# Optimization experiments

Measured on AMD Instinct MI355X. Metric: run time of the kernel, lower is better.

## Reference

```python
import jax, jax.numpy as jnp
import numpy as np

N_QUBITS = 16
DIM = 1 << N_QUBITS
NUM_CLASSES = 23
BATCH = 64

# PauliZ sign table: wire 0 is the most-significant bit of the flattened index.
_idx = np.arange(DIM)
SIGNS = np.stack([1 - 2 * ((_idx >> (N_QUBITS - 1 - w)) & 1) for w in range(N_QUBITS)], axis=1).astype(np.float32)  # (DIM, 16)


def _rx_mat(theta):
    c = jnp.cos(theta / 2).astype(jnp.complex64)
    s = (-1j * jnp.sin(theta / 2)).astype(jnp.complex64)
    return jnp.stack([jnp.stack([c, s]), jnp.stack([s, c])])  # (2,2)


def _rot_mat(phi, theta, omega):
    ct = jnp.cos(theta / 2)
    st = jnp.sin(theta / 2)
    a = jnp.exp(-0.5j * (phi + omega)) * ct
    b = -jnp.exp(0.5j * (phi - omega)) * st
    c = jnp.exp(-0.5j * (phi - omega)) * st
    d = jnp.exp(0.5j * (phi + omega)) * ct
    return jnp.stack([jnp.stack([a, b]), jnp.stack([c, d])]).astype(jnp.complex64)


def _apply_1q(state, U, w):
    # state: (B, 2,...,2); shared 2x2 gate on wire w (axis w+1)
    st = jnp.tensordot(state, U, axes=[[w + 1], [1]])  # contracted axis moves to last
    return jnp.moveaxis(st, -1, w + 1)


def _apply_rx_batched(state, theta_b, w):
    # per-sample RX angles theta_b: (B,)
    half = theta_b / 2
    c = jnp.cos(half).astype(jnp.complex64)
    s = (-1j * jnp.sin(half)).astype(jnp.complex64)
    U = jnp.stack([jnp.stack([c, s], -1), jnp.stack([s, c], -1)], -2)  # (B,2,2)
    st = jnp.moveaxis(state, w + 1, -1)
    st = jnp.einsum('bji,b...i->b...j', U, st)
    return jnp.moveaxis(st, -1, w + 1)


def _apply_crx(state, theta, ctrl, tgt):
    s0 = jax.lax.index_in_dim(state, 0, axis=ctrl + 1, keepdims=False)
    s1 = jax.lax.index_in_dim(state, 1, axis=ctrl + 1, keepdims=False)
    tax = tgt + 1 if tgt < ctrl else tgt  # target axis after control axis removal
    U = _rx_mat(theta)
    s1 = jnp.moveaxis(jnp.tensordot(s1, U, axes=[[tax], [1]]), -1, tax)
    return jnp.stack([s0, s1], axis=ctrl + 1)


def _circuit(x, w0, x0, w1, x1):
    B = x.shape[0]
    state = jnp.zeros((B,) + (2,) * N_QUBITS, jnp.complex64)
    state = state.at[(slice(None),) + (0,) * N_QUBITS].set(1.0)
    for w, xc in ((w0, x0), (w1, x1)):
        for q in range(N_QUBITS):
            state = _apply_rx_batched(state, x[:, q], q)
        for q in range(N_QUBITS):
            state = _apply_1q(state, _rot_mat(w[q, 0], w[q, 1], w[q, 2]), q)
        for q in range(N_QUBITS):
            state = _apply_crx(state, xc[q], q, (q + 1) % N_QUBITS)
    probs = (state.real ** 2 + state.imag ** 2).reshape(B, DIM)
    return probs @ jnp.asarray(SIGNS)  # (B, 16) PauliZ expvals


def setup_inputs() -> dict:
    key = jax.random.key(0)
    ks = jax.random.split(key, 7)
    return {
        'x': jax.random.normal(ks[0], (BATCH, N_QUBITS), jnp.float32),
        'w0': jax.random.normal(ks[1], (N_QUBITS, 3), jnp.float32),
        'x0': jax.random.normal(ks[2], (N_QUBITS,), jnp.float32),
        'w1': jax.random.normal(ks[3], (N_QUBITS, 3), jnp.float32),
        'x1': jax.random.normal(ks[4], (N_QUBITS,), jnp.float32),
        'fc_w': jax.random.normal(ks[5], (NUM_CLASSES, N_QUBITS), jnp.float32) * 0.25,
        'fc_b': jax.random.normal(ks[6], (NUM_CLASSES,), jnp.float32) * 0.05,
    }


def reference(x, w0, x0, w1, x1, fc_w, fc_b):
    feats = _circuit(x, w0, x0, w1, x1)           # (B, 16)
    logits = feats @ fc_w.T + fc_b                # (B, 23)
    return jax.nn.log_softmax(logits, axis=1)
```

## Files before the change

### kernel.cpp

```cpp
#include <hip/hip_runtime.h>
#include <hip/hip_bf16.h>


#define DIM 65536
#define BATCH 64
#define PSTR 580


template<int RB>
__device__ __forceinline__ void g1q_reg(float* sr, float* si, const float* U) {
  float u00r=U[0],u00i=U[1],u01r=U[2],u01i=U[3],u10r=U[4],u10i=U[5],u11r=U[6],u11i=U[7];
#pragma unroll
  for (int k = 0; k < 8; ++k) {
    int lo = k & ((1<<RB)-1);
    int j0 = ((k >> RB) << (RB+1)) | lo;
    int j1 = j0 | (1<<RB);
    float a0r=sr[j0], a0i=si[j0], a1r=sr[j1], a1i=si[j1];
    sr[j0] = u00r*a0r - u00i*a0i + u01r*a1r - u01i*a1i;
    si[j0] = u00r*a0i + u00i*a0r + u01r*a1i + u01i*a1r;
    sr[j1] = u10r*a0r - u10i*a0i + u11r*a1r - u11i*a1i;
    si[j1] = u10r*a0i + u10i*a0r + u11r*a1i + u11i*a1r;
  }
}

template<int RB, int CB>
__device__ __forceinline__ void gsel_reg_cc(float* sr, float* si, const float* M0, const float* M1) {
  float a0=M0[0],a1=M0[1],a2=M0[2],a3=M0[3],a4=M0[4],a5=M0[5],a6=M0[6],a7=M0[7];
  float b0=M1[0],b1=M1[1],b2=M1[2],b3=M1[3],b4=M1[4],b5=M1[5],b6=M1[6],b7=M1[7];
#pragma unroll
  for (int k = 0; k < 8; ++k) {
    int lo = k & ((1<<RB)-1);
    int j0 = ((k >> RB) << (RB+1)) | lo;
    int j1 = j0 | (1<<RB);
    const bool c = ((j0 >> CB) & 1) != 0;
    float u00r=c?b0:a0, u00i=c?b1:a1, u01r=c?b2:a2, u01i=c?b3:a3;
    float u10r=c?b4:a4, u10i=c?b5:a5, u11r=c?b6:a6, u11i=c?b7:a7;
    float p0r=sr[j0], p0i=si[j0], p1r=sr[j1], p1i=si[j1];
    sr[j0] = u00r*p0r - u00i*p0i + u01r*p1r - u01i*p1i;
    si[j0] = u00r*p0i + u00i*p0r + u01r*p1i + u01i*p1r;
    sr[j1] = u10r*p0r - u10i*p0i + u11r*p1r - u11i*p1i;
    si[j1] = u10r*p0i + u10i*p0r + u11r*p1i + u11i*p1r;
  }
}

template<int RB>
__device__ __forceinline__ void gsel_reg_pred(float* sr, float* si, const float* M0,
                                              const float* M1, bool ctrl) {
  float u[8];
#pragma unroll
  for (int e = 0; e < 8; ++e) u[e] = ctrl ? M1[e] : M0[e];
  g1q_reg<RB>(sr, si, u);
}

template<int CB, int LB>
__device__ __forceinline__ void crx_reg_lane(float* sr, float* si, float c, float s) {
#pragma unroll
  for (int k = 0; k < 8; ++k) {
    int lo2 = k & ((1<<CB)-1);
    int j = ((((k >> CB) << (CB+1)) | lo2)) | (1<<CB);
    float pr = __shfl_xor(sr[j], 1<<LB, 64);
    float pi = __shfl_xor(si[j], 1<<LB, 64);
    float mr = sr[j], mi = si[j];
    sr[j] = c*mr + s*pi;
    si[j] = c*mi - s*pr;
  }
}

__device__ __forceinline__ int swz(int o) { return o ^ ((o>>4)&15) ^ ((o>>8)&15); }

__device__ __forceinline__ unsigned bfp(float r, float i) {
  unsigned ur = __float_as_uint(r), ui = __float_as_uint(i);
  ur = (ur + 0x7fffu + ((ur >> 16) & 1u)) >> 16;
  ui = (ui + 0x7fffu + ((ui >> 16) & 1u)) & 0xffff0000u;
  return (ur & 0xffffu) | ui;
}
__device__ __forceinline__ float bfr(unsigned u) { return __uint_as_float(u << 16); }
__device__ __forceinline__ float bfi(unsigned u) { return __uint_as_float(u & 0xffff0000u); }

#define MP(Pb, l, q, s) ((Pb) + (((l)*16+(q))*2+(s))*8)


__global__ __launch_bounds__(512) void pB(unsigned* __restrict__ st,
                                          const float* __restrict__ x, const float* __restrict__ w0,
                                          const float* __restrict__ x0, const float* __restrict__ w1,
                                          const float* __restrict__ x1, float* __restrict__ P,
                                          float* __restrict__ feats, int* __restrict__ ctr) {
  __shared__ float2 lds2[8192];
  __shared__ float Ps[PSTR];
  int blk = blockIdx.x;
  int b = blk >> 3, m = blk & 7;
  int t = threadIdx.x, lane = t & 63, wv = t >> 6;

  {
    float (*su)[8] = reinterpret_cast<float(*)[8]>(lds2);
    if (m == 0 && t < 16) feats[b*16 + t] = 0.f;
    if (m == 0 && t == 16) ctr[b] = 0;
    if (t < 32) {
      int l = t >> 4, q = t & 15;
      const float* W = (l ? w1 : w0) + q*3;
      float xa = 0.5f * x[b*16 + q];
      float cr = cosf(xa), sx = sinf(xa);
      float phi = W[0], th = W[1], om = W[2];
      float ct = cosf(0.5f*th), stt = sinf(0.5f*th);
      float po = 0.5f*(phi+om), pm = 0.5f*(phi-om);
      float ar =  cosf(po)*ct,  ai = -sinf(po)*ct;
      float br = -cosf(pm)*stt, bi = -sinf(pm)*stt;
      float cr2 = cosf(pm)*stt, ci2 = -sinf(pm)*stt;
      float dr =  cosf(po)*ct,  di =  sinf(po)*ct;
      float U[8];
      U[0] = ar*cr + bi*sx;   U[1] = ai*cr - br*sx;
      U[2] = ai*sx + br*cr;   U[3] = -ar*sx + bi*cr;
      U[4] = cr2*cr + di*sx;  U[5] = ci2*cr - dr*sx;
      U[6] = ci2*sx + dr*cr;  U[7] = -cr2*sx + di*cr;
      float* M0 = MP(Ps, l, q, 0);
      float* M1 = M0 + 8;
#pragma unroll
      for (int e = 0; e < 8; ++e) { M0[e] = U[e]; su[t][e] = U[e]; }
      if (q == 0) {
        float ang = l ? 0.5f*x0[15] : 0.f;
        float cg = cosf(ang), sg = sinf(ang);
        M1[0] =  cg*U[0] + sg*U[3];  M1[1] = cg*U[1] - sg*U[2];
        M1[2] =  sg*U[1] + cg*U[2];  M1[3] = -sg*U[0] + cg*U[3];
        M1[4] =  cg*U[4] + sg*U[7];  M1[5] = cg*U[5] - sg*U[6];
        M1[6] =  sg*U[5] + cg*U[6];  M1[7] = -sg*U[4] + cg*U[7];
      } else {
        float ang = 0.5f*(l ? x1[q-1] : x0[q-1]);
        float cg = cosf(ang), sg = sinf(ang);
        M1[0] = cg*U[0] + sg*U[5];  M1[1] = cg*U[1] - sg*U[4];
        M1[2] = cg*U[2] + sg*U[7];  M1[3] = cg*U[3] - sg*U[6];
        M1[4] = cg*U[4] + sg*U[1];  M1[5] = cg*U[5] - sg*U[0];
        M1[6] = cg*U[6] + sg*U[3];  M1[7] = cg*U[7] - sg*U[2];
      }
      if (t == 0) { Ps[576] = cosf(0.5f*x1[15]); Ps[577] = sinf(0.5f*x1[15]); }
    }
    __syncthreads();
  }

  float sr[16], si[16];
  if (t < 256) {
#pragma unroll
    for (int r = 0; r < 16; ++r) { sr[r] = 0.f; si[r] = 0.f; }
    if (t == 0) {
      sr[0] = 1.f;
      g1q_reg<3>(sr, si, MP(Ps,0,0,0));
      gsel_reg_cc<2,3>(sr, si, MP(Ps,0,1,0), MP(Ps,0,1,1));
      gsel_reg_cc<1,2>(sr, si, MP(Ps,0,2,0), MP(Ps,0,2,1));
      gsel_reg_cc<0,1>(sr, si, MP(Ps,0,3,0), MP(Ps,0,3,1));
    }
  } else if (t < 264) {
    float (*su)[8] = reinterpret_cast<float(*)[8]>(lds2);
    int k = t - 256;
    float xr = su[13][((k>>2)&1)*4], xi = su[13][((k>>2)&1)*4+1];
    float yr = su[14][((k>>1)&1)*4], yi = su[14][((k>>1)&1)*4+1];
    float zr = su[15][(k&1)*4],      zi = su[15][(k&1)*4+1];
    float pr = xr*yr - xi*yi, pi = xr*yi + xi*yr;
    float T0r = pr*zr - pi*zi, T0i = pr*zi + pi*zr;
    float a12 = 0.5f*x0[12], c12 = cosf(a12), s12 = sinf(a12);
    float T0r4 = __shfl_xor(T0r, 4, 64), T0i4 = __shfl_xor(T0i, 4, 64);
    float T1r = c12*T0r + s12*T0i4, T1i = c12*T0i - s12*T0r4;
    float a13 = 0.5f*x0[13], c13 = cosf(a13), s13 = sinf(a13);
    float T0r2 = __shfl_xor(T0r, 2, 64), T0i2 = __shfl_xor(T0i, 2, 64);
    float T1r2 = __shfl_xor(T1r, 2, 64), T1i2 = __shfl_xor(T1i, 2, 64);
    float n0r, n0i, n1r, n1i;
    if (k & 4) {
      n0r = c13*T0r + s13*T0i2; n0i = c13*T0i - s13*T0r2;
      n1r = c13*T1r + s13*T1i2; n1i = c13*T1i - s13*T1r2;
    } else { n0r = T0r; n0i = T0i; n1r = T1r; n1i = T1i; }
    float a14 = 0.5f*x0[14], c14 = cosf(a14), s14 = sinf(a14);
    float n0r1 = __shfl_xor(n0r, 1, 64), n0i1 = __shfl_xor(n0i, 1, 64);
    float n1r1 = __shfl_xor(n1r, 1, 64), n1i1 = __shfl_xor(n1i, 1, 64);
    float F0r, F0i, F1r, F1i;
    if (k & 2) {
      F0r = c14*n0r + s14*n0i1; F0i = c14*n0i - s14*n0r1;
      F1r = c14*n1r + s14*n1i1; F1i = c14*n1i - s14*n1r1;
    } else { F0r = n0r; F0i = n0i; F1r = n1r; F1i = n1i; }
    const float* A = MP(Ps,0,12,0);
    const float* B = MP(Ps,0,12,1);
    float* T2 = Ps + 512;
#pragma unroll
    for (int j0 = 0; j0 < 2; ++j0) {
      float tr = j0 ? F1r : F0r, ti = j0 ? F1i : F0i;
#pragma unroll
      for (int j1 = 0; j1 < 2; ++j1) {
        const float* Wm = j1 ? B : A;
        float fr = Wm[j0*4], fi = Wm[j0*4+1];
        T2[((j0*2 + j1)*8 + k)*2 + 0] = tr*fr - ti*fi;
        T2[((j0*2 + j1)*8 + k)*2 + 1] = tr*fi + ti*fr;
      }
    }
  }
  __syncthreads();
  if (t < 256) {
#pragma unroll
    for (int r = 0; r < 16; ++r) {
      int o = wv | (lane << 2) | (r << 8);
      lds2[swz(o) & 4095] = make_float2(sr[r], si[r]);
    }
  }
  __syncthreads();
  if (t < 256) {
#pragma unroll
    for (int r = 0; r < 16; ++r) {
      int o = wv | (((lane>>4)&3) << 2) | (r << 4) | ((lane&15) << 8);
      float2 v = lds2[swz(o) & 4095]; sr[r] = v.x; si[r] = v.y;
    }
    if (t < 16) {
      gsel_reg_pred<3>(sr, si, MP(Ps,0,4,0), MP(Ps,0,4,1), (lane&1)!=0);
      gsel_reg_cc<2,3>(sr, si, MP(Ps,0,5,0), MP(Ps,0,5,1));
      gsel_reg_cc<1,2>(sr, si, MP(Ps,0,6,0), MP(Ps,0,6,1));
      gsel_reg_cc<0,1>(sr, si, MP(Ps,0,7,0), MP(Ps,0,7,1));
    }
  }
  __syncthreads();
  if (t < 256) {
#pragma unroll
    for (int r = 0; r < 16; ++r) {
      int o = wv | (((lane>>4)&3) << 2) | (r << 4) | ((lane&15) << 8);
      lds2[swz(o) & 4095] = make_float2(sr[r], si[r]);
    }
  }
  __syncthreads();
  if (t < 256) {
#pragma unroll
    for (int r = 0; r < 16; ++r) {
      int o = r | (lane << 4) | (wv << 10);
      float2 v = lds2[swz(o) & 4095]; sr[r] = v.x; si[r] = v.y;
    }
    gsel_reg_pred<3>(sr, si, MP(Ps,0,8,0), MP(Ps,0,8,1), (lane&1)!=0);
    gsel_reg_cc<2,3>(sr, si, MP(Ps,0,9,0), MP(Ps,0,9,1));
    gsel_reg_cc<1,2>(sr, si, MP(Ps,0,10,0), MP(Ps,0,10,1));
    gsel_reg_cc<0,1>(sr, si, MP(Ps,0,11,0), MP(Ps,0,11,1));
#pragma unroll
    for (int r = 0; r < 16; ++r) {
      int paddr = ((lane>>4)&3) | (wv << 2) | (r << 4) | ((lane&15) << 8);
      lds2[4096 + swz(paddr)] = make_float2(sr[r], si[r]);
    }
  }
  if (m == 0) {
    if (t >= 448 && t < 512) P[(size_t)b*PSTR + t] = Ps[t];
    else if (t == 320) { P[(size_t)b*PSTR + 576] = Ps[576]; P[(size_t)b*PSTR + 577] = Ps[577]; }
  }
  __syncthreads();

  {
#pragma unroll
    for (int r = 0; r < 16; ++r) {
      int paddr = r | (lane << 4) | ((wv&3) << 10);
      float2 v = lds2[4096 + swz(paddr)]; sr[r] = v.x; si[r] = v.y;
    }
    int k = ((wv>>2)&1) | ((m&3) << 1);
    const float* tf = Ps + 512 + ((((m>>2)&1)*2 + (lane&1))*8 + k)*2;
    float fr = tf[0], fi = tf[1];
    const float* M = ((wv>>2)&1) ? MP(Ps,1,0,1) : MP(Ps,1,0,0);
    float v8[8];
#pragma unroll
    for (int e = 0; e < 4; ++e) {
      v8[2*e]   = fr*M[2*e]   - fi*M[2*e+1];
      v8[2*e+1] = fr*M[2*e+1] + fi*M[2*e];
    }
    g1q_reg<3>(sr, si, v8);
  }
  gsel_reg_cc<2,3>(sr, si, MP(Ps,1,1,0), MP(Ps,1,1,1));
  gsel_reg_cc<1,2>(sr, si, MP(Ps,1,2,0), MP(Ps,1,2,1));
  gsel_reg_cc<0,1>(sr, si, MP(Ps,1,3,0), MP(Ps,1,3,1));
  __syncthreads();
#pragma unroll
  for (int r = 0; r < 16; ++r) {
    int o = (lane&63) | ((wv&3) << 6) | (r << 8) | (((wv>>2)&1) << 12);
    lds2[swz(o) & 8191] = make_float2(sr[r], si[r]);
  }
  __syncthreads();
#pragma unroll
  for (int r = 0; r < 16; ++r) {
    int o = (lane&15) | (r << 4) | (((lane>>4)&3) << 8) | ((wv&3) << 10) | (((wv>>2)&1) << 12);
    float2 v = lds2[swz(o) & 8191]; sr[r] = v.x; si[r] = v.y;
  }
  gsel_reg_pred<3>(sr, si, MP(Ps,1,4,0), MP(Ps,1,4,1), (lane&16)!=0);
  gsel_reg_cc<2,3>(sr, si, MP(Ps,1,5,0), MP(Ps,1,5,1));
  gsel_reg_cc<1,2>(sr, si, MP(Ps,1,6,0), MP(Ps,1,6,1));
  gsel_reg_cc<0,1>(sr, si, MP(Ps,1,7,0), MP(Ps,1,7,1));
  __syncthreads();
#pragma unroll
  for (int r = 0; r < 16; ++r) {
    int o = (lane&15) | (r << 4) | (((lane>>4)&3) << 8) | ((wv&3) << 10) | (((wv>>2)&1) << 12);
    lds2[swz(o) & 8191] = make_float2(sr[r], si[r]);
  }
  __syncthreads();
#pragma unroll
  for (int r = 0; r < 16; ++r) {
    int o = r | ((lane&63) << 4) | ((wv&3) << 10) | (((wv>>2)&1) << 12);
    float2 v = lds2[swz(o) & 8191]; sr[r] = v.x; si[r] = v.y;
  }
  gsel_reg_pred<3>(sr, si, MP(Ps,1,8,0), MP(Ps,1,8,1), (lane&1)!=0);
  gsel_reg_cc<2,3>(sr, si, MP(Ps,1,9,0), MP(Ps,1,9,1));
  gsel_reg_cc<1,2>(sr, si, MP(Ps,1,10,0), MP(Ps,1,10,1));
  gsel_reg_cc<0,1>(sr, si, MP(Ps,1,11,0), MP(Ps,1,11,1));
  {
    int sbase = ((lane&63) << 4) | ((wv&3) << 10) | (((wv>>2)&1) << 12) | (m << 13);
    uint4* dst = (uint4*)(st + (size_t)b*DIM + sbase);
#pragma unroll
    for (int g = 0; g < 4; ++g)
      dst[g] = make_uint4(bfp(sr[4*g],si[4*g]), bfp(sr[4*g+1],si[4*g+1]),
                          bfp(sr[4*g+2],si[4*g+2]), bfp(sr[4*g+3],si[4*g+3]));
  }
}


__global__ __launch_bounds__(512) void p3(const unsigned* __restrict__ st, const float* __restrict__ P,
                                          float* __restrict__ feats, int* __restrict__ ctr,
                                          const float* __restrict__ fcw, const float* __restrict__ fcb,
                                          float* __restrict__ out) {
  int blk = blockIdx.x;
  int b = blk >> 3, n = blk & 7;
  int t = threadIdx.x, lane = t & 63, wv = t >> 6;
  const float* Pb = P + (size_t)b*PSTR;
  int base = (lane&31) | (wv << 5) | (n << 8) | ((lane>>5) << 11);
  const unsigned* S = st + (size_t)b*DIM + base;
  float sr[16], si[16];
#pragma unroll
  for (int r = 0; r < 16; ++r) { unsigned u = S[r << 12]; sr[r] = bfr(u); si[r] = bfi(u); }

  gsel_reg_pred<3>(sr, si, MP(Pb,1,12,0), MP(Pb,1,12,1), (lane&1)!=0);
  gsel_reg_cc<2,3>(sr, si, MP(Pb,1,13,0), MP(Pb,1,13,1));
  gsel_reg_cc<1,2>(sr, si, MP(Pb,1,14,0), MP(Pb,1,14,1));
  gsel_reg_cc<0,1>(sr, si, MP(Pb,1,15,0), MP(Pb,1,15,1));
  crx_reg_lane<0,5>(sr, si, Pb[576], Pb[577]);

  float tot=0.f, sA=0.f, sB=0.f, sC=0.f, sD=0.f;
#pragma unroll
  for (int r = 0; r < 16; ++r) {
    float p = sr[r]*sr[r] + si[r]*si[r];
    tot += p;
    sA += (r & 1) ? -p : p;
    sB += (r & 2) ? -p : p;
    sC += (r & 4) ? -p : p;
    sD += (r & 8) ? -p : p;
  }
  float f[16];
  f[15] = sA; f[14] = sB; f[13] = sC; f[12] = sD;
  f[11] = (lane&1)  ? -tot : tot;
  f[10] = (lane&2)  ? -tot : tot;
  f[9]  = (lane&4)  ? -tot : tot;
  f[8]  = (lane&8)  ? -tot : tot;
  f[7]  = (lane&16) ? -tot : tot;
  f[0]  = (lane&32) ? -tot : tot;
  f[6]  = (wv&1)    ? -tot : tot;
  f[5]  = (wv&2)    ? -tot : tot;
  f[4]  = (wv&4)    ? -tot : tot;
  f[3]  = (n&1)     ? -tot : tot;
  f[2]  = (n&2)     ? -tot : tot;
  f[1]  = (n&4)     ? -tot : tot;
#pragma unroll
  for (int w = 0; w < 16; ++w) {
#pragma unroll
    for (int off = 32; off; off >>= 1) f[w] += __shfl_xor(f[w], off, 64);
  }
  __shared__ float red[8][17];
  if (lane == 0) {
#pragma unroll
    for (int w = 0; w < 16; ++w) red[wv][w] = f[w];
  }
  __syncthreads();
  if (t < 16) {
    float acc = 0.f;
#pragma unroll
    for (int i = 0; i < 8; ++i) acc += red[i][t];
    atomicAdd(&feats[b*16 + t], acc);
  }

  __shared__ int flagS;
  __syncthreads();
  if (t == 0) { __threadfence(); flagS = atomicAdd(&ctr[b], 1); }
  __syncthreads();
  if (flagS == 7) {
    __shared__ float fs[16];
    __shared__ float lg[23];
    if (t < 16) fs[t] = __hip_atomic_load(&feats[b*16 + t], __ATOMIC_RELAXED, __HIP_MEMORY_SCOPE_AGENT);
    __syncthreads();
    if (t < 23) {
      float acc = fcb[t];
#pragma unroll
      for (int w = 0; w < 16; ++w) acc += fs[w] * fcw[t*16 + w];
      lg[t] = acc;
    }
    __syncthreads();
    if (t < 23) {
      float mx = -1e30f;
#pragma unroll
      for (int j = 0; j < 23; ++j) mx = fmaxf(mx, lg[j]);
      float Ssum = 0.f;
#pragma unroll
      for (int j = 0; j < 23; ++j) Ssum += expf(lg[j] - mx);
      out[b*23 + t] = lg[t] - mx - logf(Ssum);
    }
  }
}

extern "C" void kernel_launch(void* const* d_in, const int* in_sizes, int n_in,
                              void* d_out, int out_size, void* d_ws, size_t ws_size,
                              hipStream_t stream) {
  const float* x   = (const float*)d_in[0];
  const float* w0  = (const float*)d_in[1];
  const float* x0  = (const float*)d_in[2];
  const float* w1  = (const float*)d_in[3];
  const float* x1  = (const float*)d_in[4];
  const float* fcw = (const float*)d_in[5];
  const float* fcb = (const float*)d_in[6];
  float* out = (float*)d_out;

  char* ws = (char*)d_ws;
  unsigned* st  = (unsigned*)ws;
  float*  P     = (float*)(ws + (size_t)BATCH * DIM * 4);
  float*  feats = P + (size_t)BATCH * PSTR;
  int*    ctr   = (int*)(feats + BATCH*16);

  pB<<<512, 512, 0, stream>>>(st, x, w0, x0, w1, x1, P, feats, ctr);
  p3<<<512, 512, 0, stream>>>(st, P, feats, ctr, fcw, fcb, out);
  (void)in_sizes; (void)n_in; (void)out_size; (void)ws_size;
}
```

Measured before the change: 124.4 us.

## Split first-stage kernel into 256-thread blocks covering 4K-amplitude slices each

The first-stage kernel moves from 512 blocks of 512 threads (half of them idle for the first layer) to 1024 blocks of 256 threads. Each block now owns a 4096-amplitude slice, so the shared state buffer halves and the layer-2 transposes work within that smaller slice. The first-layer work is recomputed redundantly per block instead of being spread across idle threads. The goal is to remove idle threads, cut LDS use and raise occupancy (launch_bounds 256,4). The cost is twice as much redundant per-block setup and gate-matrix computation.

```diff
diff --git a/kernel.cpp b/kernel.cpp
--- a/kernel.cpp
+++ b/kernel.cpp
@@ -80,21 +80,21 @@
 #define MP(Pb, l, q, s) ((Pb) + (((l)*16+(q))*2+(s))*8)
 
 
-__global__ __launch_bounds__(512) void pB(unsigned* __restrict__ st,
-                                          const float* __restrict__ x, const float* __restrict__ w0,
-                                          const float* __restrict__ x0, const float* __restrict__ w1,
-                                          const float* __restrict__ x1, float* __restrict__ P,
-                                          float* __restrict__ feats, int* __restrict__ ctr) {
-  __shared__ float2 lds2[8192];
+__global__ __launch_bounds__(256, 4) void pB2(unsigned* __restrict__ st,
+                                              const float* __restrict__ x, const float* __restrict__ w0,
+                                              const float* __restrict__ x0, const float* __restrict__ w1,
+                                              const float* __restrict__ x1, float* __restrict__ P,
+                                              float* __restrict__ feats, int* __restrict__ ctr) {
+  __shared__ float2 lds2[4096];
   __shared__ float Ps[PSTR];
   int blk = blockIdx.x;
-  int b = blk >> 3, m = blk & 7;
+  int b = blk >> 4, mp = blk & 15;
   int t = threadIdx.x, lane = t & 63, wv = t >> 6;
 
   {
     float (*su)[8] = reinterpret_cast<float(*)[8]>(lds2);
-    if (m == 0 && t < 16) feats[b*16 + t] = 0.f;
-    if (m == 0 && t == 16) ctr[b] = 0;
+    if (mp == 0 && t < 16) feats[b*16 + t] = 0.f;
+    if (mp == 0 && t == 16) ctr[b] = 0;
     if (t < 32) {
       int l = t >> 4, q = t & 15;
       const float* W = (l ? w1 : w0) + q*3;
@@ -137,19 +137,17 @@
   }
 
   float sr[16], si[16];
-  if (t < 256) {
-#pragma unroll
-    for (int r = 0; r < 16; ++r) { sr[r] = 0.f; si[r] = 0.f; }
-    if (t == 0) {
-      sr[0] = 1.f;
-      g1q_reg<3>(sr, si, MP(Ps,0,0,0));
-      gsel_reg_cc<2,3>(sr, si, MP(Ps,0,1,0), MP(Ps,0,1,1));
-      gsel_reg_cc<1,2>(sr, si, MP(Ps,0,2,0), MP(Ps,0,2,1));
-      gsel_reg_cc<0,1>(sr, si, MP(Ps,0,3,0), MP(Ps,0,3,1));
-    }
-  } else if (t < 264) {
+#pragma unroll
+  for (int r = 0; r < 16; ++r) { sr[r] = 0.f; si[r] = 0.f; }
+  if (t == 0) {
+    sr[0] = 1.f;
+    g1q_reg<3>(sr, si, MP(Ps,0,0,0));
+    gsel_reg_cc<2,3>(sr, si, MP(Ps,0,1,0), MP(Ps,0,1,1));
+    gsel_reg_cc<1,2>(sr, si, MP(Ps,0,2,0), MP(Ps,0,2,1));
+    gsel_reg_cc<0,1>(sr, si, MP(Ps,0,3,0), MP(Ps,0,3,1));
+  } else if (t >= 64 && t < 72) {
     float (*su)[8] = reinterpret_cast<float(*)[8]>(lds2);
-    int k = t - 256;
+    int k = t - 64;
     float xr = su[13][((k>>2)&1)*4], xi = su[13][((k>>2)&1)*4+1];
     float yr = su[14][((k>>1)&1)*4], yi = su[14][((k>>1)&1)*4+1];
     float zr = su[15][(k&1)*4],      zi = su[15][(k&1)*4+1];
@@ -189,69 +187,62 @@
       }
     }
   }
-  __syncthreads();
-  if (t < 256) {
+  if (mp == 0) {
+    if (t >= 192) P[(size_t)b*PSTR + 256 + t] = Ps[256 + t];
+    else if (t == 1) { P[(size_t)b*PSTR + 576] = Ps[576]; P[(size_t)b*PSTR + 577] = Ps[577]; }
+  }
+  __syncthreads();
+
+#pragma unroll
+  for (int r = 0; r < 16; ++r) {
+    int o = wv | (lane << 2) | (r << 8);
+    lds2[swz(o)] = make_float2(sr[r], si[r]);
+  }
+  __syncthreads();
+#pragma unroll
+  for (int r = 0; r < 16; ++r) {
+    int o = wv | (((lane>>4)&3) << 2) | (r << 4) | ((lane&15) << 8);
+    float2 v = lds2[swz(o)]; sr[r] = v.x; si[r] = v.y;
+  }
+  if (t < 16) {
+    gsel_reg_pred<3>(sr, si, MP(Ps,0,4,0), MP(Ps,0,4,1), (lane&1)!=0);
+    gsel_reg_cc<2,3>(sr, si, MP(Ps,0,5,0), MP(Ps,0,5,1));
+    gsel_reg_cc<1,2>(sr, si, MP(Ps,0,6,0), MP(Ps,0,6,1));
+    gsel_reg_cc<0,1>(sr, si, MP(Ps,0,7,0), MP(Ps,0,7,1));
+  }
+#pragma unroll
+  for (int r = 0; r < 16; ++r) {
+    int o = wv | (((lane>>4)&3) << 2) | (r << 4) | ((lane&15) << 8);
+    lds2[swz(o)] = make_float2(sr[r], si[r]);
+  }
+  __syncthreads();
+#pragma unroll
+  for (int r = 0; r < 16; ++r) {
+    int o = r | (lane << 4) | (wv << 10);
+    float2 v = lds2[swz(o)]; sr[r] = v.x; si[r] = v.y;
+  }
+  gsel_reg_pred<3>(sr, si, MP(Ps,0,8,0), MP(Ps,0,8,1), (lane&1)!=0);
+  gsel_reg_cc<2,3>(sr, si, MP(Ps,0,9,0), MP(Ps,0,9,1));
+  gsel_reg_cc<1,2>(sr, si, MP(Ps,0,10,0), MP(Ps,0,10,1));
+  gsel_reg_cc<0,1>(sr, si, MP(Ps,0,11,0), MP(Ps,0,11,1));
+  __syncthreads();
+#pragma unroll
+  for (int r = 0; r < 16; ++r) {
+    int paddr = ((lane>>4)&3) | (wv << 2) | (r << 4) | ((lane&15) << 8);
+    lds2[swz(paddr)] = make_float2(sr[r], si[r]);
+  }
+  __syncthreads();
+
+  {
 #pragma unroll
     for (int r = 0; r < 16; ++r) {
-      int o = wv | (lane << 2) | (r << 8);
-      lds2[swz(o) & 4095] = make_float2(sr[r], si[r]);
-    }
-  }
-  __syncthreads();
-  if (t < 256) {
-#pragma unroll
-    for (int r = 0; r < 16; ++r) {
-      int o = wv | (((lane>>4)&3) << 2) | (r << 4) | ((lane&15) << 8);
-      float2 v = lds2[swz(o) & 4095]; sr[r] = v.x; si[r] = v.y;
-    }
-    if (t < 16) {
-      gsel_reg_pred<3>(sr, si, MP(Ps,0,4,0), MP(Ps,0,4,1), (lane&1)!=0);
-      gsel_reg_cc<2,3>(sr, si, MP(Ps,0,5,0), MP(Ps,0,5,1));
-      gsel_reg_cc<1,2>(sr, si, MP(Ps,0,6,0), MP(Ps,0,6,1));
-      gsel_reg_cc<0,1>(sr, si, MP(Ps,0,7,0), MP(Ps,0,7,1));
-    }
-  }
-  __syncthreads();
-  if (t < 256) {
-#pragma unroll
-    for (int r = 0; r < 16; ++r) {
-      int o = wv | (((lane>>4)&3) << 2) | (r << 4) | ((lane&15) << 8);
-      lds2[swz(o) & 4095] = make_float2(sr[r], si[r]);
-    }
-  }
-  __syncthreads();
-  if (t < 256) {
-#pragma unroll
-    for (int r = 0; r < 16; ++r) {
-      int o = r | (lane << 4) | (wv << 10);
-      float2 v = lds2[swz(o) & 4095]; sr[r] = v.x; si[r] = v.y;
-    }
-    gsel_reg_pred<3>(sr, si, MP(Ps,0,8,0), MP(Ps,0,8,1), (lane&1)!=0);
-    gsel_reg_cc<2,3>(sr, si, MP(Ps,0,9,0), MP(Ps,0,9,1));
-    gsel_reg_cc<1,2>(sr, si, MP(Ps,0,10,0), MP(Ps,0,10,1));
-    gsel_reg_cc<0,1>(sr, si, MP(Ps,0,11,0), MP(Ps,0,11,1));
-#pragma unroll
-    for (int r = 0; r < 16; ++r) {
-      int paddr = ((lane>>4)&3) | (wv << 2) | (r << 4) | ((lane&15) << 8);
-      lds2[4096 + swz(paddr)] = make_float2(sr[r], si[r]);
-    }
-  }
-  if (m == 0) {
-    if (t >= 448 && t < 512) P[(size_t)b*PSTR + t] = Ps[t];
-    else if (t == 320) { P[(size_t)b*PSTR + 576] = Ps[576]; P[(size_t)b*PSTR + 577] = Ps[577]; }
-  }
-  __syncthreads();
-
-  {
-#pragma unroll
-    for (int r = 0; r < 16; ++r) {
-      int paddr = r | (lane << 4) | ((wv&3) << 10);
-      float2 v = lds2[4096 + swz(paddr)]; sr[r] = v.x; si[r] = v.y;
-    }
-    int k = ((wv>>2)&1) | ((m&3) << 1);
-    const float* tf = Ps + 512 + ((((m>>2)&1)*2 + (lane&1))*8 + k)*2;
+      int paddr = r | (lane << 4) | (wv << 10);
+      float2 v = lds2[swz(paddr)]; sr[r] = v.x; si[r] = v.y;
+    }
+    int k = mp & 7;
+    const float* tf = Ps + 512 + (((((mp>>3)&1)*2 + (lane&1))*8 + k)*2);
     float fr = tf[0], fi = tf[1];
-    const float* M = ((wv>>2)&1) ? MP(Ps,1,0,1) : MP(Ps,1,0,0);
+    const float* M = (mp&1) ? MP(Ps,1,0,1) : MP(Ps,1,0,0);
     float v8[8];
 #pragma unroll
     for (int e = 0; e < 4; ++e) {
@@ -266,37 +257,36 @@
   __syncthreads();
 #pragma unroll
   for (int r = 0; r < 16; ++r) {
-    int o = (lane&63) | ((wv&3) << 6) | (r << 8) | (((wv>>2)&1) << 12);
-    lds2[swz(o) & 8191] = make_float2(sr[r], si[r]);
-  }
-  __syncthreads();
-#pragma unroll
-  for (int r = 0; r < 16; ++r) {
-    int o = (lane&15) | (r << 4) | (((lane>>4)&3) << 8) | ((wv&3) << 10) | (((wv>>2)&1) << 12);
-    float2 v = lds2[swz(o) & 8191]; sr[r] = v.x; si[r] = v.y;
-  }
-  gsel_reg_pred<3>(sr, si, MP(Ps,1,4,0), MP(Ps,1,4,1), (lane&16)!=0);
+    int o = lane | (wv << 6) | (r << 8);
+    lds2[swz(o)] = make_float2(sr[r], si[r]);
+  }
+  __syncthreads();
+#pragma unroll
+  for (int r = 0; r < 16; ++r) {
+    int o = wv | (((lane>>4)&3) << 2) | (r << 4) | ((lane&15) << 8);
+    float2 v = lds2[swz(o)]; sr[r] = v.x; si[r] = v.y;
+  }
+  gsel_reg_pred<3>(sr, si, MP(Ps,1,4,0), MP(Ps,1,4,1), (lane&1)!=0);
   gsel_reg_cc<2,3>(sr, si, MP(Ps,1,5,0), MP(Ps,1,5,1));
   gsel_reg_cc<1,2>(sr, si, MP(Ps,1,6,0), MP(Ps,1,6,1));
   gsel_reg_cc<0,1>(sr, si, MP(Ps,1,7,0), MP(Ps,1,7,1));
-  __syncthreads();
-#pragma unroll
-  for (int r = 0; r < 16; ++r) {
-    int o = (lane&15) | (r << 4) | (((lane>>4)&3) << 8) | ((wv&3) << 10) | (((wv>>2)&1) << 12);
-    lds2[swz(o) & 8191] = make_float2(sr[r], si[r]);
-  }
-  __syncthreads();
-#pragma unroll
-  for (int r = 0; r < 16; ++r) {
-    int o = r | ((lane&63) << 4) | ((wv&3) << 10) | (((wv>>2)&1) << 12);
-    float2 v = lds2[swz(o) & 8191]; sr[r] = v.x; si[r] = v.y;
+#pragma unroll
+  for (int r = 0; r < 16; ++r) {
+    int o = wv | (((lane>>4)&3) << 2) | (r << 4) | ((lane&15) << 8);
+    lds2[swz(o)] = make_float2(sr[r], si[r]);
+  }
+  __syncthreads();
+#pragma unroll
+  for (int r = 0; r < 16; ++r) {
+    int o = r | (lane << 4) | (wv << 10);
+    float2 v = lds2[swz(o)]; sr[r] = v.x; si[r] = v.y;
   }
   gsel_reg_pred<3>(sr, si, MP(Ps,1,8,0), MP(Ps,1,8,1), (lane&1)!=0);
   gsel_reg_cc<2,3>(sr, si, MP(Ps,1,9,0), MP(Ps,1,9,1));
   gsel_reg_cc<1,2>(sr, si, MP(Ps,1,10,0), MP(Ps,1,10,1));
   gsel_reg_cc<0,1>(sr, si, MP(Ps,1,11,0), MP(Ps,1,11,1));
   {
-    int sbase = ((lane&63) << 4) | ((wv&3) << 10) | (((wv>>2)&1) << 12) | (m << 13);
+    int sbase = (lane << 4) | (wv << 10) | (mp << 12);
     uint4* dst = (uint4*)(st + (size_t)b*DIM + sbase);
 #pragma unroll
     for (int g = 0; g < 4; ++g)
@@ -414,7 +404,7 @@
   float*  feats = P + (size_t)BATCH * PSTR;
   int*    ctr   = (int*)(feats + BATCH*16);
 
-  pB<<<512, 512, 0, stream>>>(st, x, w0, x0, w1, x1, P, feats, ctr);
+  pB2<<<1024, 256, 0, stream>>>(st, x, w0, x0, w1, x1, P, feats, ctr);
   p3<<<512, 512, 0, stream>>>(st, P, feats, ctr, fcw, fcb, out);
   (void)in_sizes; (void)n_in; (void)out_size; (void)ws_size;
 }
```

New measurement: 129.2 us. 1.04x slower.
